# Optimization experiments

Measured on AMD Instinct MI355X. Metric: run time of the kernel, lower is better.

## Reference

```python
import jax, jax.numpy as jnp
import numpy as np

EPS_ATTN = 1e-8  # self.eps is undefined in the torch source; standard slot-attention value
LN_EPS = 1e-5


def _ln(x, g=None, b=None, axes=(-1,)):
    m = x.mean(axes, keepdims=True)
    v = ((x - m) ** 2).mean(axes, keepdims=True)
    y = (x - m) * jax.lax.rsqrt(v + LN_EPS)
    return y * g + b if g is not None else y


def setup_inputs() -> dict:
    key = jax.random.key(0)
    ks = jax.random.split(key, 16)
    B, N, S, d, dh = 16, 4096, 8, 64, 128

    def w(k, shape, fan_in):
        return jax.random.normal(k, shape, jnp.float32) / np.float32(np.sqrt(fan_in))

    return {
        "inputs": jax.random.normal(ks[0], (B, N, d + 2), jnp.float32),
        "slots": jax.random.normal(ks[1], (S, d + 4), jnp.float32),
        "Wq": w(ks[2], (d, d), d),
        "Wk": w(ks[3], (d, d), d),
        "Wv": w(ks[4], (d, d), d),
        "Wg": w(ks[5], (d, 2), 2),
        "bg": jnp.zeros((d,), jnp.float32),
        "ln_pos_g": jnp.ones((d,), jnp.float32),
        "ln_pos_b": jnp.zeros((d,), jnp.float32),
        "W1": w(ks[6], (dh, d), d),
        "b1": jnp.zeros((dh,), jnp.float32),
        "W2": w(ks[7], (d, dh), dh),
        "b2": jnp.zeros((d,), jnp.float32),
        "W_ih": w(ks[8], (3 * d, d), d),
        "W_hh": w(ks[9], (3 * d, d), d),
        "b_ih": jnp.zeros((3 * d,), jnp.float32),
        "b_hh": jnp.zeros((3 * d,), jnp.float32),
        "ln_mlp_g": jnp.ones((d,), jnp.float32),
        "ln_mlp_b": jnp.zeros((d,), jnp.float32),
        "W3": w(ks[10], (dh, d), d),
        "b3": jnp.zeros((dh,), jnp.float32),
        "W4": w(ks[11], (d, dh), dh),
        "b4": jnp.zeros((d,), jnp.float32),
        "ln_slot_g": jnp.ones((d,), jnp.float32),
        "ln_slot_b": jnp.zeros((d,), jnp.float32),
        "n_iters": 3,
    }


def reference(inputs, slots, Wq, Wk, Wv, Wg, bg, ln_pos_g, ln_pos_b, W1, b1, W2, b2,
              W_ih, W_hh, b_ih, b_hh, ln_mlp_g, ln_mlp_b, W3, b3, W4, b4,
              ln_slot_g, ln_slot_b, n_iters):
    feats, grids = inputs[..., :-2], inputs[..., -2:]          # (B,N,d), (B,N,2)
    sl, pos, sc = slots[..., :-4], slots[..., -4:-2], slots[..., -2:]
    B, N, _ = feats.shape
    S, d = sl.shape
    scale = d ** (-0.5)

    slots = jnp.broadcast_to(sl, (B, S, d))
    positions = jnp.clip(jnp.broadcast_to(pos, (B, S, 2)), -1.0, 1.0)
    scales = jnp.clip(jnp.broadcast_to(sc, (B, S, 2)), 1e-3, 2.0)

    k = feats @ Wk.T                                           # (B,N,d)
    v = feats @ Wv.T

    def pos_mlp(x):  # LayerNorm -> Linear -> ReLU -> Linear
        h = _ln(x, ln_pos_g, ln_pos_b)
        h = jax.nn.relu(h @ W1.T + b1)
        return h @ W2.T + b2

    for i_iter in range(n_iters + 1):
        rel = (grids[:, :, None] - positions[:, None]) / scales[:, None]  # (B,N,S,2)
        rgp = rel @ Wg.T + bg                                             # (B,N,S,d)
        k_pos = pos_mlp(k[:, :, None] + rgp)                              # (B,N,S,d)
        v_pos = pos_mlp(v[:, :, None] + rgp)

        slots_n = _ln(slots, ln_slot_g, ln_slot_b)
        q = _ln(slots_n, axes=(-2, -1)) @ Wq.T                            # (B,S,d)

        dots = jnp.einsum('bsd,bnsd->bns', q, k_pos) * scale              # (B,N,S)
        attn = jax.nn.softmax(dots, axis=1) + EPS_ATTN
        attn = attn / attn.sum(axis=-1, keepdims=True)

        updates = jnp.einsum('bns,bnsd->bsd', attn, v_pos)                # (B,S,d)
        positions = jnp.einsum('bns,bnp->bsp', attn, grids)               # (B,S,2)
        spread = (grids[:, :, None] - positions[:, None]) ** 2            # (B,N,S,2)
        scales = jnp.clip(jnp.sqrt(jnp.einsum('bns,bnsp->bsp', attn, spread)), 1e-3, 2.0)

        if i_iter < n_iters:
            x = updates.reshape(-1, d)
            h = slots.reshape(-1, d)
            gi = x @ W_ih.T + b_ih
            gh = h @ W_hh.T + b_hh
            i_r, i_z, i_n = jnp.split(gi, 3, axis=-1)
            h_r, h_z, h_n = jnp.split(gh, 3, axis=-1)
            r = jax.nn.sigmoid(i_r + h_r)
            z = jax.nn.sigmoid(i_z + h_z)
            n_g = jnp.tanh(i_n + r * h_n)
            slots = ((1.0 - z) * n_g + z * h).reshape(B, S, d)
            # slot_mlp (no residual in the source)
            hmlp = jax.nn.relu(_ln(slots, ln_mlp_g, ln_mlp_b) @ W3.T + b3)
            slots = hmlp @ W4.T + b4

    return jnp.concatenate([slots, positions, scales], axis=-1)           # (B,S,d+4)
```

## Files before the change

### kernel.cpp

```cpp
#include <hip/hip_runtime.h>
#include <math.h>

#define BB 16
#define NN 4096
#define SS 8
#define DD 64
#define DHH 128
#define CIN 66
#define NITERS 3
#define LN_EPS_F 1e-5f
#define EPS_ATTN_F 1e-8f
#define QSCALE 0.125f

__device__ __forceinline__ float dot4(float4 a, float4 b) {
    return fmaf(a.x, b.x, fmaf(a.y, b.y, fmaf(a.z, b.z, a.w * b.w)));
}

__global__ __launch_bounds__(256) void k_init_slots(
    const float* __restrict__ slots_in, float* __restrict__ slots,
    float* __restrict__ positions, float* __restrict__ scales) {
    int tid = blockIdx.x * 256 + threadIdx.x;
    if (tid < BB * SS * DD) {
        int s = (tid / DD) % SS;
        int c = tid % DD;
        slots[tid] = slots_in[s * 68 + c];
    }
    if (tid < BB * SS * 2) {
        int s = (tid >> 1) & 7;
        int p = tid & 1;
        float po = slots_in[s * 68 + 64 + p];
        positions[tid] = fminf(fmaxf(po, -1.f), 1.f);
        float sc = slots_in[s * 68 + 66 + p];
        scales[tid] = fminf(fmaxf(sc, 1e-3f), 2.f);
    }
}

__global__ __launch_bounds__(256) void k_prep_w(
    const float* __restrict__ W1, const float* __restrict__ lpg,
    const float* __restrict__ lpb, const float* __restrict__ b1,
    const float* __restrict__ Wg,
    float* __restrict__ W1p, float* __restrict__ avec, float* __restrict__ bvec,
    float* __restrict__ s1vec, float* __restrict__ b1p, float* __restrict__ wgc) {
    __shared__ float w1s[128 * 68];
    int tid = threadIdx.x;
    for (int q = 0; q < 8; q++) {
        int flat = q * 1024 + tid * 4;
        int o = flat >> 6, c = flat & 63;
        *(float4*)(w1s + o * 68 + c) = *(const float4*)(W1 + flat);
    }
    __syncthreads();
    if (tid < 128) {
        int o = tid;
        float a = 0.f, bv = 0.f, s1 = 0.f, b1a = b1[o];
        for (int c = 0; c < 64; c++) {
            float w0 = w1s[o * 68 + c];
            float w = w0 * lpg[c];
            W1p[o * 64 + c] = w;
            a = fmaf(w, Wg[2 * c], a);
            bv = fmaf(w, Wg[2 * c + 1], bv);
            s1 += w;
            b1a = fmaf(w0, lpb[c], b1a);
        }
        avec[o] = a; bvec[o] = bv; s1vec[o] = s1; b1p[o] = b1a;
    }
    if (tid == 128) {
        float mwA = 0.f, mwB = 0.f, AA = 0.f, BBv = 0.f, AB = 0.f;
        for (int c = 0; c < 64; c++) {
            float wa = Wg[2 * c], wb = Wg[2 * c + 1];
            mwA += wa; mwB += wb;
            AA = fmaf(wa, wa, AA); BBv = fmaf(wb, wb, BBv); AB = fmaf(wa, wb, AB);
        }
        wgc[0] = mwA * (1.f / 64.f);
        wgc[1] = mwB * (1.f / 64.f);
        wgc[2] = AA * (1.f / 64.f);
        wgc[3] = BBv * (1.f / 64.f);
        wgc[4] = AB * (2.f / 64.f);
    }
}

__global__ __launch_bounds__(256) void k_prep_w2(
    const float* __restrict__ W1p, const float* __restrict__ Wk,
    const float* __restrict__ Wv, const float* __restrict__ bg,
    float* __restrict__ Wall, float* __restrict__ cu) {
    int flat = blockIdx.x * 256 + threadIdx.x;
    int mat = flat >> 13, rem = flat & 8191;
    int o = rem >> 6, c = rem & 63;
    const float* Wm = mat ? Wv : Wk;
    float acc = 0.f;
    for (int d = 0; d < 64; d++)
        acc = fmaf(W1p[o * 64 + d], Wm[d * 64 + c], acc);
    Wall[flat] = acc;
    if (flat < 128) {
        float a = 0.f;
        for (int d = 0; d < 64; d++) a = fmaf(W1p[flat * 64 + d], bg[d], a);
        cu[flat] = a;
    }
}

__global__ __launch_bounds__(256) void k_prep_main(
    const float* __restrict__ inp, const float* __restrict__ Wall,
    const float* __restrict__ cu, const float* __restrict__ Wk,
    const float* __restrict__ Wv, const float* __restrict__ bg,
    const float* __restrict__ Wg,
    float* __restrict__ uk, float* __restrict__ uv,
    float* __restrict__ kaux, float* __restrict__ vaux, float* __restrict__ gbuf) {
    __shared__ float A[64 * 68];
    __shared__ float Bw[128 * 68];
    __shared__ float wg2[132];
    __shared__ float bgs[64];
    __shared__ float cus[128];
    int tid = threadIdx.x;
    int chunk = blockIdx.y;
    int rowBase = blockIdx.x * 64;
    {
        int r = tid >> 2, cq = (tid & 3) * 16;
        const float* src = inp + (size_t)(rowBase + r) * CIN + cq;
        float* dst = A + r * 68 + cq;
        #pragma unroll
        for (int q = 0; q < 8; q++) {
            float2 tv = *(const float2*)(src + 2 * q);
            dst[2 * q] = tv.x; dst[2 * q + 1] = tv.y;
        }
    }
    if (chunk < 2) {
        const float* Wsrc = Wall + (size_t)chunk * 8192;
        int o = tid >> 1, c0 = (tid & 1) * 32;
        #pragma unroll
        for (int q = 0; q < 8; q++)
            *(float4*)(Bw + o * 68 + c0 + 4 * q) = *(const float4*)(Wsrc + o * 64 + c0 + 4 * q);
        if (tid < 128) cus[tid] = cu[tid];
    } else {
        int o = tid >> 1, c0 = (tid & 1) * 32;
        const float* Wsrc = (o < 64) ? (Wk + o * 64) : (Wv + (o - 64) * 64);
        #pragma unroll
        for (int q = 0; q < 8; q++)
            *(float4*)(Bw + o * 68 + c0 + 4 * q) = *(const float4*)(Wsrc + c0 + 4 * q);
        if (tid < 64) {
            wg2[tid] = Wg[2 * tid]; wg2[66 + tid] = Wg[2 * tid + 1];
            bgs[tid] = bg[tid];
        }
    }
    __syncthreads();
    int r2 = tid >> 3, j = tid & 7;
    float acc0[16], acc1[16];
    #pragma unroll
    for (int q = 0; q < 16; q++) { acc0[q] = 0.f; acc1[q] = 0.f; }
    for (int c4 = 0; c4 < 64; c4 += 4) {
        float4 a0 = *(const float4*)(A + r2 * 68 + c4);
        float4 a1 = *(const float4*)(A + (r2 + 32) * 68 + c4);
        #pragma unroll
        for (int q = 0; q < 16; q++) {
            float4 w = *(const float4*)(Bw + (8 * q + j) * 68 + c4);
            acc0[q] += dot4(a0, w);
            acc1[q] += dot4(a1, w);
        }
    }
    if (chunk < 2) {
        float cub[16];
        #pragma unroll
        for (int q = 0; q < 16; q++) cub[q] = cus[8 * q + j];
        __syncthreads();
        #pragma unroll
        for (int q = 0; q < 16; q++) {
            Bw[r2 * 132 + 8 * q + j] = acc0[q] + cub[q];
            Bw[(r2 + 32) * 132 + 8 * q + j] = acc1[q] + cub[q];
        }
        __syncthreads();
        float* dst = (chunk == 0) ? uk : uv;
        int r = tid >> 2, c0 = (tid & 3) * 32;
        #pragma unroll
        for (int q = 0; q < 8; q++)
            *(float4*)(dst + (size_t)(rowBase + r) * 128 + c0 + 4 * q) =
                *(const float4*)(Bw + r * 132 + c0 + 4 * q);
    } else {
        float mk[2] = {0.f, 0.f}, kk[2] = {0.f, 0.f}, kA[2] = {0.f, 0.f}, kB[2] = {0.f, 0.f};
        float mv[2] = {0.f, 0.f}, vv[2] = {0.f, 0.f}, vA[2] = {0.f, 0.f}, vB[2] = {0.f, 0.f};
        #pragma unroll
        for (int q = 0; q < 8; q++) {
            int ch = 8 * q + j;
            float bgv = bgs[ch], wa = wg2[ch], wb = wg2[66 + ch];
            float x0 = acc0[q] + bgv, x1 = acc1[q] + bgv;
            mk[0] += x0; kk[0] = fmaf(x0, x0, kk[0]); kA[0] = fmaf(x0, wa, kA[0]); kB[0] = fmaf(x0, wb, kB[0]);
            mk[1] += x1; kk[1] = fmaf(x1, x1, kk[1]); kA[1] = fmaf(x1, wa, kA[1]); kB[1] = fmaf(x1, wb, kB[1]);
            float y0 = acc0[q + 8] + bgv, y1 = acc1[q + 8] + bgv;
            mv[0] += y0; vv[0] = fmaf(y0, y0, vv[0]); vA[0] = fmaf(y0, wa, vA[0]); vB[0] = fmaf(y0, wb, vB[0]);
            mv[1] += y1; vv[1] = fmaf(y1, y1, vv[1]); vA[1] = fmaf(y1, wa, vA[1]); vB[1] = fmaf(y1, wb, vB[1]);
        }
        #pragma unroll
        for (int off = 1; off <= 4; off <<= 1) {
            #pragma unroll
            for (int rr = 0; rr < 2; rr++) {
                mk[rr] += __shfl_xor(mk[rr], off, 64); kk[rr] += __shfl_xor(kk[rr], off, 64);
                kA[rr] += __shfl_xor(kA[rr], off, 64); kB[rr] += __shfl_xor(kB[rr], off, 64);
                mv[rr] += __shfl_xor(mv[rr], off, 64); vv[rr] += __shfl_xor(vv[rr], off, 64);
                vA[rr] += __shfl_xor(vA[rr], off, 64); vB[rr] += __shfl_xor(vB[rr], off, 64);
            }
        }
        if (j == 0) {
            #pragma unroll
            for (int rr = 0; rr < 2; rr++) {
                int row = rowBase + r2 + rr * 32;
                float g0 = inp[(size_t)row * CIN + 64];
                float g1 = inp[(size_t)row * CIN + 65];
                float4 m1 = {mk[rr] * (1.f / 64.f), kk[rr] * (1.f / 64.f),
                             kA[rr] * (1.f / 32.f), kB[rr] * (1.f / 32.f)};
                float4 m2 = {g0, g1, 0.f, 0.f};
                *(float4*)(kaux + (size_t)row * 8) = m1;
                *(float4*)(kaux + (size_t)row * 8 + 4) = m2;
                float4 n1 = {mv[rr] * (1.f / 64.f), vv[rr] * (1.f / 64.f),
                             vA[rr] * (1.f / 32.f), vB[rr] * (1.f / 32.f)};
                *(float4*)(vaux + (size_t)row * 8) = n1;
                *(float4*)(vaux + (size_t)row * 8 + 4) = m2;
                *(float2*)(gbuf + (size_t)row * 2) = {g0, g1};
            }
        }
    }
}

__global__ __launch_bounds__(512) void k_slot_prep(
    const float* __restrict__ slots, const float* __restrict__ lsg,
    const float* __restrict__ lsb, const float* __restrict__ Wq,
    const float* __restrict__ W2, const float* __restrict__ b2,
    float* __restrict__ w2q, float* __restrict__ qb2) {
    __shared__ float sn[512];
    __shared__ float qv[SS][64];
    __shared__ float wsum[8], wsum2[8];
    int b = blockIdx.x, t = threadIdx.x;
    int s = t >> 6, c = t & 63;
    float x = slots[(b * SS + s) * DD + c];
    float sum = x;
    for (int off = 32; off; off >>= 1) sum += __shfl_xor(sum, off, 64);
    float m = sum * (1.f / 64.f);
    float dv = x - m;
    float vs = dv * dv;
    for (int off = 32; off; off >>= 1) vs += __shfl_xor(vs, off, 64);
    float y = dv * rsqrtf(vs * (1.f / 64.f) + LN_EPS_F) * lsg[c] + lsb[c];
    float s1 = y, s2 = y * y;
    for (int off = 32; off; off >>= 1) { s1 += __shfl_xor(s1, off, 64); s2 += __shfl_xor(s2, off, 64); }
    if (c == 0) { wsum[s] = s1; wsum2[s] = s2; }
    __syncthreads();
    float ts1 = 0.f, ts2 = 0.f;
    #pragma unroll
    for (int i = 0; i < 8; i++) { ts1 += wsum[i]; ts2 += wsum2[i]; }
    float gm = ts1 * (1.f / 512.f);
    float gv = ts2 * (1.f / 512.f) - gm * gm;
    sn[t] = (y - gm) * rsqrtf(gv + LN_EPS_F);
    __syncthreads();
    float acc = 0.f;
    for (int j4 = 0; j4 < 64; j4 += 4)
        acc += dot4(*(const float4*)&sn[s * 64 + j4], *(const float4*)(Wq + c * 64 + j4));
    qv[s][c] = acc;
    __syncthreads();
    float a0 = 0.f, a1 = 0.f;
    for (int cc = 0; cc < 64; cc++) {
        float qc = qv[s][cc];
        a0 = fmaf(qc, W2[cc * DHH + c], a0);
        a1 = fmaf(qc, W2[cc * DHH + c + 64], a1);
    }
    w2q[(b * SS + s) * DHH + c] = a0 * QSCALE;
    w2q[(b * SS + s) * DHH + c + 64] = a1 * QSCALE;
    float qb = qv[s][c] * b2[c];
    for (int off = 32; off; off >>= 1) qb += __shfl_xor(qb, off, 64);
    if (c == 0) qb2[b * SS + s] = qb * QSCALE;
}

__global__ __launch_bounds__(256) void k_pass1(
    const float* __restrict__ uk, const float* __restrict__ kaux,
    const float* __restrict__ positions, const float* __restrict__ scales,
    const float* __restrict__ avec, const float* __restrict__ bvec,
    const float* __restrict__ s1vec, const float* __restrict__ b1p,
    const float* __restrict__ wgc, const float* __restrict__ w2q,
    const float* __restrict__ qb2, float* __restrict__ dots) {
    int tid = threadIdx.x;
    int chunk = blockIdx.x, b = blockIdx.y;
    int wv = tid >> 6, lane = tid & 63, rh = lane >> 5, ol = lane & 31;
    int o4 = ol * 4;
    float4 a4 = *(const float4*)(avec + o4);
    float4 bv4 = *(const float4*)(bvec + o4);
    float4 s14 = *(const float4*)(s1vec + o4);
    float4 b14 = *(const float4*)(b1p + o4);
    float mwA = wgc[0], mwB = wgc[1], AA = wgc[2], BBc = wgc[3], AB2 = wgc[4];
    float p0[8], p1[8], rc0[8], rc1[8], qb[8];
    float4 wq[8];
    #pragma unroll
    for (int s = 0; s < 8; s++) {
        int bs = b * 8 + s;
        p0[s] = positions[bs * 2]; p1[s] = positions[bs * 2 + 1];
        rc0[s] = 1.f / scales[bs * 2]; rc1[s] = 1.f / scales[bs * 2 + 1];
        qb[s] = qb2[bs];
        wq[s] = *(const float4*)(w2q + (size_t)bs * DHH + o4);
    }
    int row0 = chunk * 64 + wv * 16 + rh;
    size_t rg = (size_t)b * NN + row0;
    float4 m1 = *(const float4*)(kaux + rg * 8);
    float4 m2 = *(const float4*)(kaux + rg * 8 + 4);
    float4 u4 = *(const float4*)(uk + rg * 128 + o4);
    for (int st = 0; st < 8; st++) {
        float4 n1, n2, nu;
        if (st < 7) {
            size_t rgn = rg + (size_t)(st + 1) * 2;
            n1 = *(const float4*)(kaux + rgn * 8);
            n2 = *(const float4*)(kaux + rgn * 8 + 4);
            nu = *(const float4*)(uk + rgn * 128 + o4);
        }
        int row = row0 + st * 2;
        #pragma unroll
        for (int s = 0; s < 8; s++) {
            float rel0 = (m2.x - p0[s]) * rc0[s];
            float rel1 = (m2.y - p1[s]) * rc1[s];
            float m = fmaf(rel1, mwB, fmaf(rel0, mwA, m1.x));
            float q2 = fmaf(rel0, fmaf(rel0, AA, m1.z), m1.y);
            q2 = fmaf(rel1, fmaf(rel1, BBc, m1.w), q2);
            q2 = fmaf(rel0 * rel1, AB2, q2);
            float var = fmaf(-m, m, q2);
            float rstd = rsqrtf(fmaxf(var, 0.f) + LN_EPS_F);
            float p = 0.f, t, h;
            t = fmaf(-m, s14.x, u4.x); t = fmaf(rel0, a4.x, t); t = fmaf(rel1, bv4.x, t);
            h = fmaf(rstd, t, b14.x); p = fmaf(fmaxf(h, 0.f), wq[s].x, p);
            t = fmaf(-m, s14.y, u4.y); t = fmaf(rel0, a4.y, t); t = fmaf(rel1, bv4.y, t);
            h = fmaf(rstd, t, b14.y); p = fmaf(fmaxf(h, 0.f), wq[s].y, p);
            t = fmaf(-m, s14.z, u4.z); t = fmaf(rel0, a4.z, t); t = fmaf(rel1, bv4.z, t);
            h = fmaf(rstd, t, b14.z); p = fmaf(fmaxf(h, 0.f), wq[s].z, p);
            t = fmaf(-m, s14.w, u4.w); t = fmaf(rel0, a4.w, t); t = fmaf(rel1, bv4.w, t);
            h = fmaf(rstd, t, b14.w); p = fmaf(fmaxf(h, 0.f), wq[s].w, p);
            p += __shfl_xor(p, 1, 64);
            p += __shfl_xor(p, 2, 64);
            p += __shfl_xor(p, 4, 64);
            p += __shfl_xor(p, 8, 64);
            p += __shfl_xor(p, 16, 64);
            if (ol == 0)
                dots[(size_t)(b * 8 + s) * NN + row] = p + qb[s];
        }
        m1 = n1; m2 = n2; u4 = nu;
    }
}

__global__ __launch_bounds__(256) void k_pass2(
    const float* __restrict__ uv, const float* __restrict__ vaux,
    const float* __restrict__ positions, const float* __restrict__ scales,
    const float* __restrict__ avec, const float* __restrict__ bvec,
    const float* __restrict__ s1vec, const float* __restrict__ b1p,
    const float* __restrict__ wgc, const float* __restrict__ attn,
    float* __restrict__ H) {
    __shared__ float Hw[4 * 1024];
    int tid = threadIdx.x;
    int chunk = blockIdx.x, b = blockIdx.y;
    int wv = tid >> 6, lane = tid & 63, rh = lane >> 5, ol = lane & 31;
    int o4 = ol * 4;
    float4 a4 = *(const float4*)(avec + o4);
    float4 bv4 = *(const float4*)(bvec + o4);
    float4 s14 = *(const float4*)(s1vec + o4);
    float4 b14 = *(const float4*)(b1p + o4);
    float mwA = wgc[0], mwB = wgc[1], AA = wgc[2], BBc = wgc[3], AB2 = wgc[4];
    float p0[8], p1[8], rc0[8], rc1[8];
    #pragma unroll
    for (int s = 0; s < 8; s++) {
        int bs = b * 8 + s;
        p0[s] = positions[bs * 2]; p1[s] = positions[bs * 2 + 1];
        rc0[s] = 1.f / scales[bs * 2]; rc1[s] = 1.f / scales[bs * 2 + 1];
    }
    float hq[8][4];
    #pragma unroll
    for (int s = 0; s < 8; s++)
        #pragma unroll
        for (int c = 0; c < 4; c++) hq[s][c] = 0.f;
    int row0 = chunk * 64 + wv * 16 + rh;
    size_t rg = (size_t)b * NN + row0;
    float4 m1 = *(const float4*)(vaux + rg * 8);
    float4 m2 = *(const float4*)(vaux + rg * 8 + 4);
    float4 u4 = *(const float4*)(uv + rg * 128 + o4);
    for (int st = 0; st < 8; st++) {
        float4 n1, n2, nu;
        if (st < 7) {
            size_t rgn = rg + (size_t)(st + 1) * 2;
            n1 = *(const float4*)(vaux + rgn * 8);
            n2 = *(const float4*)(vaux + rgn * 8 + 4);
            nu = *(const float4*)(uv + rgn * 128 + o4);
        }
        int row = row0 + st * 2;
        #pragma unroll
        for (int s = 0; s < 8; s++) {
            float ar = attn[(size_t)(b * 8 + s) * NN + row];
            float rel0 = (m2.x - p0[s]) * rc0[s];
            float rel1 = (m2.y - p1[s]) * rc1[s];
            float m = fmaf(rel1, mwB, fmaf(rel0, mwA, m1.x));
            float q2 = fmaf(rel0, fmaf(rel0, AA, m1.z), m1.y);
            q2 = fmaf(rel1, fmaf(rel1, BBc, m1.w), q2);
            q2 = fmaf(rel0 * rel1, AB2, q2);
            float var = fmaf(-m, m, q2);
            float rstd = rsqrtf(fmaxf(var, 0.f) + LN_EPS_F);
            float t, h;
            t = fmaf(-m, s14.x, u4.x); t = fmaf(rel0, a4.x, t); t = fmaf(rel1, bv4.x, t);
            h = fmaf(rstd, t, b14.x); hq[s][0] = fmaf(ar, fmaxf(h, 0.f), hq[s][0]);
            t = fmaf(-m, s14.y, u4.y); t = fmaf(rel0, a4.y, t); t = fmaf(rel1, bv4.y, t);
            h = fmaf(rstd, t, b14.y); hq[s][1] = fmaf(ar, fmaxf(h, 0.f), hq[s][1]);
            t = fmaf(-m, s14.z, u4.z); t = fmaf(rel0, a4.z, t); t = fmaf(rel1, bv4.z, t);
            h = fmaf(rstd, t, b14.z); hq[s][2] = fmaf(ar, fmaxf(h, 0.f), hq[s][2]);
            t = fmaf(-m, s14.w, u4.w); t = fmaf(rel0, a4.w, t); t = fmaf(rel1, bv4.w, t);
            h = fmaf(rstd, t, b14.w); hq[s][3] = fmaf(ar, fmaxf(h, 0.f), hq[s][3]);
        }
        m1 = n1; m2 = n2; u4 = nu;
    }
    #pragma unroll
    for (int s = 0; s < 8; s++)
        #pragma unroll
        for (int c = 0; c < 4; c++)
            hq[s][c] += __shfl_xor(hq[s][c], 32, 64);
    if (lane < 32) {
        #pragma unroll
        for (int s = 0; s < 8; s++) {
            float4 st = {hq[s][0], hq[s][1], hq[s][2], hq[s][3]};
            *(float4*)(Hw + wv * 1024 + s * 128 + o4) = st;
        }
    }
    __syncthreads();
    #pragma unroll
    for (int q = 0; q < 4; q++) {
        int flat = q * 256 + tid;
        float sum = Hw[flat] + Hw[1024 + flat] + Hw[2048 + flat] + Hw[3072 + flat];
        atomicAdd(&H[(size_t)b * 8 * DHH + flat], sum);
    }
}

__global__ __launch_bounds__(256) void k_softmax_ms(
    const float* __restrict__ dots, float* __restrict__ Mv, float* __restrict__ Lv,
    float* __restrict__ H) {
    __shared__ float red[4];
    int bs = blockIdx.x, t = threadIdx.x;
    if (t < 128) H[(size_t)bs * DHH + t] = 0.f;
    const float* dp = dots + (size_t)bs * NN;
    float mx = -1e30f;
    #pragma unroll
    for (int it = 0; it < 4; it++) {
        float4 d = *(const float4*)(dp + it * 1024 + t * 4);
        mx = fmaxf(mx, fmaxf(fmaxf(d.x, d.y), fmaxf(d.z, d.w)));
    }
    for (int off = 32; off; off >>= 1) mx = fmaxf(mx, __shfl_xor(mx, off, 64));
    if ((t & 63) == 0) red[t >> 6] = mx;
    __syncthreads();
    float M = fmaxf(fmaxf(red[0], red[1]), fmaxf(red[2], red[3]));
    __syncthreads();
    float sm = 0.f;
    #pragma unroll
    for (int it = 0; it < 4; it++) {
        float4 d = *(const float4*)(dp + it * 1024 + t * 4);
        sm += expf(d.x - M) + expf(d.y - M) + expf(d.z - M) + expf(d.w - M);
    }
    for (int off = 32; off; off >>= 1) sm += __shfl_xor(sm, off, 64);
    if ((t & 63) == 0) red[t >> 6] = sm;
    __syncthreads();
    if (t == 0) { Mv[bs] = M; Lv[bs] = red[0] + red[1] + red[2] + red[3]; }
}

__global__ __launch_bounds__(256) void k_attn(
    const float* __restrict__ dots, const float* __restrict__ Mv,
    const float* __restrict__ Lv, float* __restrict__ attn) {
    int chunk = blockIdx.x, b = blockIdx.y;
    int n = chunk * 256 + threadIdx.x;
    float a[8];
    float rs = 0.f;
    #pragma unroll
    for (int s = 0; s < 8; s++) {
        int bs = b * 8 + s;
        float d = dots[(size_t)bs * NN + n];
        a[s] = expf(d - Mv[bs]) * (1.f / Lv[bs]) + EPS_ATTN_F;
        rs += a[s];
    }
    float inv = 1.f / rs;
    #pragma unroll
    for (int s = 0; s < 8; s++)
        attn[(size_t)(b * 8 + s) * NN + n] = a[s] * inv;
}

__global__ __launch_bounds__(256) void k_stats(
    const float* __restrict__ attn, const float* __restrict__ gbuf,
    float* __restrict__ positions, float* __restrict__ scales,
    float* __restrict__ stats) {
    __shared__ float red[4][5];
    int bs = blockIdx.x, b = bs >> 3, t = threadIdx.x;
    const float* ap = attn + (size_t)bs * NN;
    const float* gb = gbuf + (size_t)b * NN * 2;
    float v0 = 0.f, v1 = 0.f, v2 = 0.f, v3 = 0.f, v4 = 0.f;
    #pragma unroll
    for (int it = 0; it < 4; it++) {
        int n0 = it * 1024 + t * 4;
        float4 av = *(const float4*)(ap + n0);
        float4 g1 = *(const float4*)(gb + (size_t)n0 * 2);
        float4 g2 = *(const float4*)(gb + (size_t)n0 * 2 + 4);
        v0 += av.x + av.y + av.z + av.w;
        v1 = fmaf(av.x, g1.x, fmaf(av.y, g1.z, fmaf(av.z, g2.x, fmaf(av.w, g2.z, v1))));
        v2 = fmaf(av.x, g1.y, fmaf(av.y, g1.w, fmaf(av.z, g2.y, fmaf(av.w, g2.w, v2))));
        v3 = fmaf(av.x, g1.x * g1.x, fmaf(av.y, g1.z * g1.z, fmaf(av.z, g2.x * g2.x, fmaf(av.w, g2.z * g2.z, v3))));
        v4 = fmaf(av.x, g1.y * g1.y, fmaf(av.y, g1.w * g1.w, fmaf(av.z, g2.y * g2.y, fmaf(av.w, g2.w * g2.w, v4))));
    }
    for (int off = 32; off; off >>= 1) {
        v0 += __shfl_xor(v0, off, 64); v1 += __shfl_xor(v1, off, 64);
        v2 += __shfl_xor(v2, off, 64); v3 += __shfl_xor(v3, off, 64);
        v4 += __shfl_xor(v4, off, 64);
    }
    if ((t & 63) == 0) {
        int w = t >> 6;
        red[w][0] = v0; red[w][1] = v1; red[w][2] = v2; red[w][3] = v3; red[w][4] = v4;
    }
    __syncthreads();
    if (t == 0) {
        float A0 = red[0][0] + red[1][0] + red[2][0] + red[3][0];
        float A1x = red[0][1] + red[1][1] + red[2][1] + red[3][1];
        float A1y = red[0][2] + red[1][2] + red[2][2] + red[3][2];
        float A2x = red[0][3] + red[1][3] + red[2][3] + red[3][3];
        float A2y = red[0][4] + red[1][4] + red[2][4] + red[3][4];
        positions[bs * 2 + 0] = A1x;
        positions[bs * 2 + 1] = A1y;
        float sx = A2x - A1x * A1x * (2.f - A0);
        float sy = A2y - A1y * A1y * (2.f - A0);
        scales[bs * 2 + 0] = fminf(fmaxf(sqrtf(fmaxf(sx, 0.f)), 1e-3f), 2.f);
        scales[bs * 2 + 1] = fminf(fmaxf(sqrtf(fmaxf(sy, 0.f)), 1e-3f), 2.f);
        stats[bs] = A0;
    }
}

__global__ __launch_bounds__(64) void k_gru_mlp(
    const float* __restrict__ H, const float* __restrict__ stats,
    const float* __restrict__ W2, const float* __restrict__ b2,
    const float* __restrict__ W_ih, const float* __restrict__ W_hh,
    const float* __restrict__ b_ih, const float* __restrict__ b_hh,
    const float* __restrict__ lmg, const float* __restrict__ lmb,
    const float* __restrict__ W3, const float* __restrict__ b3,
    const float* __restrict__ W4, const float* __restrict__ b4,
    float* __restrict__ slots) {
    int bs = blockIdx.x;
    int c = threadIdx.x;
    __shared__ float hl[DHH], ul[DD], sl[DD], yl[DD], hml[DHH];
    hl[c] = H[bs * DHH + c];
    hl[c + 64] = H[bs * DHH + 64 + c];
    float hold = slots[bs * DD + c];
    sl[c] = hold;
    __syncthreads();
    float A0 = stats[bs];
    float u = A0 * b2[c];
    for (int o = 0; o < DHH; o += 4) {
        float4 w = *(const float4*)(W2 + c * DHH + o);
        u = fmaf(w.x, hl[o], fmaf(w.y, hl[o + 1], fmaf(w.z, hl[o + 2], fmaf(w.w, hl[o + 3], u))));
    }
    ul[c] = u;
    __syncthreads();
    float gir = b_ih[c], giz = b_ih[64 + c], gin = b_ih[128 + c];
    float ghr = b_hh[c], ghz = b_hh[64 + c], ghn = b_hh[128 + c];
    for (int k4 = 0; k4 < DD; k4 += 4) {
        float4 uu = *(const float4*)(ul + k4);
        float4 hh = *(const float4*)(sl + k4);
        gir += dot4(uu, *(const float4*)(W_ih + c * DD + k4));
        giz += dot4(uu, *(const float4*)(W_ih + (64 + c) * DD + k4));
        gin += dot4(uu, *(const float4*)(W_ih + (128 + c) * DD + k4));
        ghr += dot4(hh, *(const float4*)(W_hh + c * DD + k4));
        ghz += dot4(hh, *(const float4*)(W_hh + (64 + c) * DD + k4));
        ghn += dot4(hh, *(const float4*)(W_hh + (128 + c) * DD + k4));
    }
    float rg = 1.f / (1.f + expf(-(gir + ghr)));
    float zg = 1.f / (1.f + expf(-(giz + ghz)));
    float ng = tanhf(gin + rg * ghn);
    float snew = (1.f - zg) * ng + zg * hold;
    float sum = snew;
    for (int off = 32; off; off >>= 1) sum += __shfl_xor(sum, off, 64);
    float m = sum * (1.f / 64.f);
    float dv = snew - m;
    float vv = dv * dv;
    for (int off = 32; off; off >>= 1) vv += __shfl_xor(vv, off, 64);
    yl[c] = dv * rsqrtf(vv * (1.f / 64.f) + LN_EPS_F) * lmg[c] + lmb[c];
    __syncthreads();
    float h0 = b3[c], h1 = b3[64 + c];
    for (int k4 = 0; k4 < DD; k4 += 4) {
        float4 yy = *(const float4*)(yl + k4);
        h0 += dot4(yy, *(const float4*)(W3 + c * DD + k4));
        h1 += dot4(yy, *(const float4*)(W3 + (64 + c) * DD + k4));
    }
    hml[c] = fmaxf(h0, 0.f);
    hml[64 + c] = fmaxf(h1, 0.f);
    __syncthreads();
    float outv = b4[c];
    for (int o4 = 0; o4 < DHH; o4 += 4) {
        float4 hm4 = *(const float4*)(hml + o4);
        outv += dot4(hm4, *(const float4*)(W4 + c * DHH + o4));
    }
    slots[bs * DD + c] = outv;
}

__global__ __launch_bounds__(256) void k_write_out(
    const float* __restrict__ slots, const float* __restrict__ positions,
    const float* __restrict__ scales, float* __restrict__ out) {
    int tid = blockIdx.x * 256 + threadIdx.x;
    if (tid >= BB * SS * 68) return;
    int bs = tid / 68, c = tid % 68;
    float v;
    if (c < 64) v = slots[bs * 64 + c];
    else if (c < 66) v = positions[bs * 2 + (c - 64)];
    else v = scales[bs * 2 + (c - 66)];
    out[tid] = v;
}

extern "C" void kernel_launch(void* const* d_in, const int* in_sizes, int n_in,
                              void* d_out, int out_size, void* d_ws, size_t ws_size,
                              hipStream_t stream) {
    (void)in_sizes; (void)n_in; (void)out_size; (void)ws_size;
    const float* inp = (const float*)d_in[0];
    const float* slots_in = (const float*)d_in[1];
    const float* Wq = (const float*)d_in[2];
    const float* Wk = (const float*)d_in[3];
    const float* Wv = (const float*)d_in[4];
    const float* Wg = (const float*)d_in[5];
    const float* bg = (const float*)d_in[6];
    const float* lpg = (const float*)d_in[7];
    const float* lpb = (const float*)d_in[8];
    const float* W1 = (const float*)d_in[9];
    const float* b1 = (const float*)d_in[10];
    const float* W2 = (const float*)d_in[11];
    const float* b2 = (const float*)d_in[12];
    const float* W_ih = (const float*)d_in[13];
    const float* W_hh = (const float*)d_in[14];
    const float* b_ih = (const float*)d_in[15];
    const float* b_hh = (const float*)d_in[16];
    const float* lmg = (const float*)d_in[17];
    const float* lmb = (const float*)d_in[18];
    const float* W3 = (const float*)d_in[19];
    const float* b3 = (const float*)d_in[20];
    const float* W4 = (const float*)d_in[21];
    const float* b4 = (const float*)d_in[22];
    const float* lsg = (const float*)d_in[23];
    const float* lsb = (const float*)d_in[24];
    float* out = (float*)d_out;
    float* ws = (float*)d_ws;

    const size_t NR = (size_t)BB * NN;
    size_t o_uk = 0;
    size_t o_uv = o_uk + NR * 128;
    size_t o_kaux = o_uv + NR * 128;
    size_t o_vaux = o_kaux + NR * 8;
    size_t o_gbuf = o_vaux + NR * 8;
    size_t o_dots = o_gbuf + NR * 2;
    size_t o_attn = o_dots + NR * SS;
    size_t o_slots = o_attn + NR * SS;
    size_t o_pos = o_slots + BB * SS * DD;
    size_t o_scl = o_pos + BB * SS * 2;
    size_t o_w2q = o_scl + BB * SS * 2;
    size_t o_qb2 = o_w2q + BB * SS * DHH;
    size_t o_Mv = o_qb2 + BB * SS;
    size_t o_Lv = o_Mv + BB * SS;
    size_t o_H = o_Lv + BB * SS;
    size_t o_stats = o_H + BB * SS * DHH;
    size_t o_W1p = o_stats + BB * SS;
    size_t o_avec = o_W1p + DHH * DD;
    size_t o_bvec = o_avec + DHH;
    size_t o_s1v = o_bvec + DHH;
    size_t o_b1p = o_s1v + DHH;
    size_t o_wgc = o_b1p + DHH;
    size_t o_Wall = o_wgc + 8;
    size_t o_cu = o_Wall + 2 * DHH * DD;

    float* uk = ws + o_uk;
    float* uv = ws + o_uv;
    float* kaux = ws + o_kaux;
    float* vaux = ws + o_vaux;
    float* gbuf = ws + o_gbuf;
    float* dots = ws + o_dots;
    float* attn = ws + o_attn;
    float* slots = ws + o_slots;
    float* positions = ws + o_pos;
    float* scales = ws + o_scl;
    float* w2q = ws + o_w2q;
    float* qb2 = ws + o_qb2;
    float* Mv = ws + o_Mv;
    float* Lv = ws + o_Lv;
    float* H = ws + o_H;
    float* stats = ws + o_stats;
    float* W1p = ws + o_W1p;
    float* avec = ws + o_avec;
    float* bvec = ws + o_bvec;
    float* s1v = ws + o_s1v;
    float* b1p = ws + o_b1p;
    float* wgc = ws + o_wgc;
    float* Wall = ws + o_Wall;
    float* cu = ws + o_cu;

    k_init_slots<<<32, 256, 0, stream>>>(slots_in, slots, positions, scales);
    k_prep_w<<<1, 256, 0, stream>>>(W1, lpg, lpb, b1, Wg, W1p, avec, bvec, s1v, b1p, wgc);
    k_prep_w2<<<64, 256, 0, stream>>>(W1p, Wk, Wv, bg, Wall, cu);
    k_prep_main<<<dim3(1024, 3), 256, 0, stream>>>(inp, Wall, cu, Wk, Wv, bg, Wg,
                                                   uk, uv, kaux, vaux, gbuf);

    for (int it = 0; it <= NITERS; ++it) {
        k_slot_prep<<<BB, 512, 0, stream>>>(slots, lsg, lsb, Wq, W2, b2, w2q, qb2);
        k_pass1<<<dim3(64, BB), 256, 0, stream>>>(uk, kaux, positions, scales,
                                                  avec, bvec, s1v, b1p, wgc, w2q, qb2, dots);
        k_softmax_ms<<<BB * SS, 256, 0, stream>>>(dots, Mv, Lv, H);
        k_attn<<<dim3(16, BB), 256, 0, stream>>>(dots, Mv, Lv, attn);
        if (it < NITERS) {
            k_pass2<<<dim3(64, BB), 256, 0, stream>>>(uv, vaux, positions, scales,
                                                      avec, bvec, s1v, b1p, wgc, attn, H);
            k_stats<<<BB * SS, 256, 0, stream>>>(attn, gbuf, positions, scales, stats);
            k_gru_mlp<<<BB * SS, 64, 0, stream>>>(H, stats, W2, b2, W_ih, W_hh, b_ih, b_hh,
                                                  lmg, lmb, W3, b3, W4, b4, slots);
        } else {
            k_stats<<<BB * SS, 256, 0, stream>>>(attn, gbuf, positions, scales, stats);
        }
    }
    k_write_out<<<34, 256, 0, stream>>>(slots, positions, scales, out);
}
```

Before: 474.9 us.

## Fuse attention normalization, stats and slot prep into pass2 and GRU kernels

Drops the separate attention-materialization and stats kernels. Pass2 now recomputes normalized attention from dots plus the softmax max and sum, and accumulates position statistics directly. The GRU/MLP kernel is merged with slot prep into one block per batch that also computes positions and scales. Pass1 and prep_main get new thread mappings (one slot per lane group, 8x8 register tiles with 128 threads). Together this cuts kernel launches and global traffic for the attn and gbuf buffers, at the cost of more complex kernels and a different reduction order.

```diff
diff --git a/kernel.cpp b/kernel.cpp
--- a/kernel.cpp
+++ b/kernel.cpp
@@ -97,14 +97,14 @@
     }
 }
 
-__global__ __launch_bounds__(256) void k_prep_main(
+__global__ __launch_bounds__(128) void k_prep_main(
     const float* __restrict__ inp, const float* __restrict__ Wall,
     const float* __restrict__ cu, const float* __restrict__ Wk,
     const float* __restrict__ Wv, const float* __restrict__ bg,
     const float* __restrict__ Wg,
     float* __restrict__ uk, float* __restrict__ uv,
-    float* __restrict__ kaux, float* __restrict__ vaux, float* __restrict__ gbuf) {
-    __shared__ float A[64 * 68];
+    float* __restrict__ kaux, float* __restrict__ vaux) {
+    __shared__ float A[64 * 66];
     __shared__ float Bw[128 * 68];
     __shared__ float wg2[132];
     __shared__ float bgs[64];
@@ -113,105 +113,105 @@
     int chunk = blockIdx.y;
     int rowBase = blockIdx.x * 64;
     {
-        int r = tid >> 2, cq = (tid & 3) * 16;
-        const float* src = inp + (size_t)(rowBase + r) * CIN + cq;
-        float* dst = A + r * 68 + cq;
-        #pragma unroll
-        for (int q = 0; q < 8; q++) {
+        int r = tid >> 1, half = tid & 1;
+        const float* src = inp + (size_t)(rowBase + r) * CIN + half * 32;
+        float* dst = A + r * 66 + half * 32;
+        #pragma unroll
+        for (int q = 0; q < 16; q++) {
             float2 tv = *(const float2*)(src + 2 * q);
             dst[2 * q] = tv.x; dst[2 * q + 1] = tv.y;
         }
     }
     if (chunk < 2) {
-        const float* Wsrc = Wall + (size_t)chunk * 8192;
-        int o = tid >> 1, c0 = (tid & 1) * 32;
-        #pragma unroll
-        for (int q = 0; q < 8; q++)
-            *(float4*)(Bw + o * 68 + c0 + 4 * q) = *(const float4*)(Wsrc + o * 64 + c0 + 4 * q);
-        if (tid < 128) cus[tid] = cu[tid];
+        const float* Wsrc = Wall + (size_t)chunk * 8192 + tid * 64;
+        float* dst = Bw + tid * 68;
+        #pragma unroll
+        for (int q = 0; q < 16; q++)
+            *(float4*)(dst + 4 * q) = *(const float4*)(Wsrc + 4 * q);
+        cus[tid] = cu[tid];
     } else {
-        int o = tid >> 1, c0 = (tid & 1) * 32;
-        const float* Wsrc = (o < 64) ? (Wk + o * 64) : (Wv + (o - 64) * 64);
-        #pragma unroll
-        for (int q = 0; q < 8; q++)
-            *(float4*)(Bw + o * 68 + c0 + 4 * q) = *(const float4*)(Wsrc + c0 + 4 * q);
+        const float* Wsrc = (tid < 64) ? (Wk + tid * 64) : (Wv + (tid - 64) * 64);
+        float* dst = Bw + tid * 68;
+        #pragma unroll
+        for (int q = 0; q < 16; q++)
+            *(float4*)(dst + 4 * q) = *(const float4*)(Wsrc + 4 * q);
         if (tid < 64) {
             wg2[tid] = Wg[2 * tid]; wg2[66 + tid] = Wg[2 * tid + 1];
             bgs[tid] = bg[tid];
         }
     }
     __syncthreads();
-    int r2 = tid >> 3, j = tid & 7;
-    float acc0[16], acc1[16];
-    #pragma unroll
-    for (int q = 0; q < 16; q++) { acc0[q] = 0.f; acc1[q] = 0.f; }
+    int oj = tid & 15, rg = tid >> 4;
+    float acc[8][8];
+    #pragma unroll
+    for (int rr = 0; rr < 8; rr++)
+        #pragma unroll
+        for (int q = 0; q < 8; q++) acc[rr][q] = 0.f;
     for (int c4 = 0; c4 < 64; c4 += 4) {
-        float4 a0 = *(const float4*)(A + r2 * 68 + c4);
-        float4 a1 = *(const float4*)(A + (r2 + 32) * 68 + c4);
-        #pragma unroll
-        for (int q = 0; q < 16; q++) {
-            float4 w = *(const float4*)(Bw + (8 * q + j) * 68 + c4);
-            acc0[q] += dot4(a0, w);
-            acc1[q] += dot4(a1, w);
+        float4 av[8];
+        #pragma unroll
+        for (int rr = 0; rr < 8; rr++)
+            av[rr] = *(const float4*)(A + (rg + 8 * rr) * 66 + c4);
+        #pragma unroll
+        for (int q = 0; q < 8; q++) {
+            float4 w = *(const float4*)(Bw + (q * 16 + oj) * 68 + c4);
+            #pragma unroll
+            for (int rr = 0; rr < 8; rr++) acc[rr][q] += dot4(av[rr], w);
         }
     }
     if (chunk < 2) {
-        float cub[16];
-        #pragma unroll
-        for (int q = 0; q < 16; q++) cub[q] = cus[8 * q + j];
+        float cub[8];
+        #pragma unroll
+        for (int q = 0; q < 8; q++) cub[q] = cus[q * 16 + oj];
         __syncthreads();
         #pragma unroll
-        for (int q = 0; q < 16; q++) {
-            Bw[r2 * 132 + 8 * q + j] = acc0[q] + cub[q];
-            Bw[(r2 + 32) * 132 + 8 * q + j] = acc1[q] + cub[q];
-        }
+        for (int rr = 0; rr < 8; rr++)
+            #pragma unroll
+            for (int q = 0; q < 8; q++)
+                Bw[(rg + 8 * rr) * 132 + q * 16 + oj] = acc[rr][q] + cub[q];
         __syncthreads();
         float* dst = (chunk == 0) ? uk : uv;
-        int r = tid >> 2, c0 = (tid & 3) * 32;
-        #pragma unroll
-        for (int q = 0; q < 8; q++)
-            *(float4*)(dst + (size_t)(rowBase + r) * 128 + c0 + 4 * q) =
-                *(const float4*)(Bw + r * 132 + c0 + 4 * q);
+        int r = tid >> 1, half = tid & 1;
+        #pragma unroll
+        for (int q = 0; q < 16; q++)
+            *(float4*)(dst + (size_t)(rowBase + r) * 128 + half * 64 + 4 * q) =
+                *(const float4*)(Bw + r * 132 + half * 64 + 4 * q);
     } else {
-        float mk[2] = {0.f, 0.f}, kk[2] = {0.f, 0.f}, kA[2] = {0.f, 0.f}, kB[2] = {0.f, 0.f};
-        float mv[2] = {0.f, 0.f}, vv[2] = {0.f, 0.f}, vA[2] = {0.f, 0.f}, vB[2] = {0.f, 0.f};
-        #pragma unroll
-        for (int q = 0; q < 8; q++) {
-            int ch = 8 * q + j;
-            float bgv = bgs[ch], wa = wg2[ch], wb = wg2[66 + ch];
-            float x0 = acc0[q] + bgv, x1 = acc1[q] + bgv;
-            mk[0] += x0; kk[0] = fmaf(x0, x0, kk[0]); kA[0] = fmaf(x0, wa, kA[0]); kB[0] = fmaf(x0, wb, kB[0]);
-            mk[1] += x1; kk[1] = fmaf(x1, x1, kk[1]); kA[1] = fmaf(x1, wa, kA[1]); kB[1] = fmaf(x1, wb, kB[1]);
-            float y0 = acc0[q + 8] + bgv, y1 = acc1[q + 8] + bgv;
-            mv[0] += y0; vv[0] = fmaf(y0, y0, vv[0]); vA[0] = fmaf(y0, wa, vA[0]); vB[0] = fmaf(y0, wb, vB[0]);
-            mv[1] += y1; vv[1] = fmaf(y1, y1, vv[1]); vA[1] = fmaf(y1, wa, vA[1]); vB[1] = fmaf(y1, wb, vB[1]);
-        }
-        #pragma unroll
-        for (int off = 1; off <= 4; off <<= 1) {
+        float wa[4], wb[4], bgk[4];
+        #pragma unroll
+        for (int q = 0; q < 4; q++) {
+            int ch = q * 16 + oj;
+            wa[q] = wg2[ch]; wb[q] = wg2[66 + ch]; bgk[q] = bgs[ch];
+        }
+        #pragma unroll
+        for (int rr = 0; rr < 8; rr++) {
+            float mk = 0.f, kk = 0.f, kA = 0.f, kB = 0.f;
+            float mv = 0.f, vv = 0.f, vA = 0.f, vB = 0.f;
             #pragma unroll
-            for (int rr = 0; rr < 2; rr++) {
-                mk[rr] += __shfl_xor(mk[rr], off, 64); kk[rr] += __shfl_xor(kk[rr], off, 64);
-                kA[rr] += __shfl_xor(kA[rr], off, 64); kB[rr] += __shfl_xor(kB[rr], off, 64);
-                mv[rr] += __shfl_xor(mv[rr], off, 64); vv[rr] += __shfl_xor(vv[rr], off, 64);
-                vA[rr] += __shfl_xor(vA[rr], off, 64); vB[rr] += __shfl_xor(vB[rr], off, 64);
+            for (int q = 0; q < 4; q++) {
+                float x = acc[rr][q] + bgk[q];
+                mk += x; kk = fmaf(x, x, kk); kA = fmaf(x, wa[q], kA); kB = fmaf(x, wb[q], kB);
+                float y = acc[rr][q + 4] + bgk[q];
+                mv += y; vv = fmaf(y, y, vv); vA = fmaf(y, wa[q], vA); vB = fmaf(y, wb[q], vB);
             }
-        }
-        if (j == 0) {
             #pragma unroll
-            for (int rr = 0; rr < 2; rr++) {
-                int row = rowBase + r2 + rr * 32;
+            for (int off = 1; off <= 8; off <<= 1) {
+                mk += __shfl_xor(mk, off, 64); kk += __shfl_xor(kk, off, 64);
+                kA += __shfl_xor(kA, off, 64); kB += __shfl_xor(kB, off, 64);
+                mv += __shfl_xor(mv, off, 64); vv += __shfl_xor(vv, off, 64);
+                vA += __shfl_xor(vA, off, 64); vB += __shfl_xor(vB, off, 64);
+            }
+            if (oj == 0) {
+                int row = rowBase + rg + 8 * rr;
                 float g0 = inp[(size_t)row * CIN + 64];
                 float g1 = inp[(size_t)row * CIN + 65];
-                float4 m1 = {mk[rr] * (1.f / 64.f), kk[rr] * (1.f / 64.f),
-                             kA[rr] * (1.f / 32.f), kB[rr] * (1.f / 32.f)};
+                float4 m1 = {mk * (1.f / 64.f), kk * (1.f / 64.f), kA * (1.f / 32.f), kB * (1.f / 32.f)};
                 float4 m2 = {g0, g1, 0.f, 0.f};
                 *(float4*)(kaux + (size_t)row * 8) = m1;
                 *(float4*)(kaux + (size_t)row * 8 + 4) = m2;
-                float4 n1 = {mv[rr] * (1.f / 64.f), vv[rr] * (1.f / 64.f),
-                             vA[rr] * (1.f / 32.f), vB[rr] * (1.f / 32.f)};
+                float4 n1 = {mv * (1.f / 64.f), vv * (1.f / 64.f), vA * (1.f / 32.f), vB * (1.f / 32.f)};
                 *(float4*)(vaux + (size_t)row * 8) = n1;
                 *(float4*)(vaux + (size_t)row * 8 + 4) = m2;
-                *(float2*)(gbuf + (size_t)row * 2) = {g0, g1};
             }
         }
     }
@@ -272,67 +272,97 @@
     const float* __restrict__ wgc, const float* __restrict__ w2q,
     const float* __restrict__ qb2, float* __restrict__ dots) {
     int tid = threadIdx.x;
-    int chunk = blockIdx.x, b = blockIdx.y;
-    int wv = tid >> 6, lane = tid & 63, rh = lane >> 5, ol = lane & 31;
-    int o4 = ol * 4;
-    float4 a4 = *(const float4*)(avec + o4);
-    float4 bv4 = *(const float4*)(bvec + o4);
-    float4 s14 = *(const float4*)(s1vec + o4);
-    float4 b14 = *(const float4*)(b1p + o4);
+    int wv = tid >> 6, lane = tid & 63;
+    int s = lane >> 3, cg = lane & 7, c0 = cg * 16;
+    int b = blockIdx.y, bs = b * SS + s;
+    float4 a4[4], bv4[4], s14[4], b14[4], wq4[4];
+    #pragma unroll
+    for (int k = 0; k < 4; k++) {
+        a4[k] = *(const float4*)(avec + c0 + 4 * k);
+        bv4[k] = *(const float4*)(bvec + c0 + 4 * k);
+        s14[k] = *(const float4*)(s1vec + c0 + 4 * k);
+        b14[k] = *(const float4*)(b1p + c0 + 4 * k);
+        wq4[k] = *(const float4*)(w2q + (size_t)bs * DHH + c0 + 4 * k);
+    }
+    float p0 = positions[bs * 2], p1 = positions[bs * 2 + 1];
+    float rc0 = 1.f / scales[bs * 2], rc1 = 1.f / scales[bs * 2 + 1];
+    float qb = qb2[bs];
     float mwA = wgc[0], mwB = wgc[1], AA = wgc[2], BBc = wgc[3], AB2 = wgc[4];
-    float p0[8], p1[8], rc0[8], rc1[8], qb[8];
-    float4 wq[8];
-    #pragma unroll
-    for (int s = 0; s < 8; s++) {
-        int bs = b * 8 + s;
-        p0[s] = positions[bs * 2]; p1[s] = positions[bs * 2 + 1];
-        rc0[s] = 1.f / scales[bs * 2]; rc1[s] = 1.f / scales[bs * 2 + 1];
-        qb[s] = qb2[bs];
-        wq[s] = *(const float4*)(w2q + (size_t)bs * DHH + o4);
-    }
-    int row0 = chunk * 64 + wv * 16 + rh;
-    size_t rg = (size_t)b * NN + row0;
-    float4 m1 = *(const float4*)(kaux + rg * 8);
-    float4 m2 = *(const float4*)(kaux + rg * 8 + 4);
-    float4 u4 = *(const float4*)(uk + rg * 128 + o4);
-    for (int st = 0; st < 8; st++) {
-        float4 n1, n2, nu;
-        if (st < 7) {
-            size_t rgn = rg + (size_t)(st + 1) * 2;
-            n1 = *(const float4*)(kaux + rgn * 8);
-            n2 = *(const float4*)(kaux + rgn * 8 + 4);
-            nu = *(const float4*)(uk + rgn * 128 + o4);
-        }
-        int row = row0 + st * 2;
-        #pragma unroll
-        for (int s = 0; s < 8; s++) {
-            float rel0 = (m2.x - p0[s]) * rc0[s];
-            float rel1 = (m2.y - p1[s]) * rc1[s];
-            float m = fmaf(rel1, mwB, fmaf(rel0, mwA, m1.x));
-            float q2 = fmaf(rel0, fmaf(rel0, AA, m1.z), m1.y);
-            q2 = fmaf(rel1, fmaf(rel1, BBc, m1.w), q2);
-            q2 = fmaf(rel0 * rel1, AB2, q2);
-            float var = fmaf(-m, m, q2);
-            float rstd = rsqrtf(fmaxf(var, 0.f) + LN_EPS_F);
-            float p = 0.f, t, h;
-            t = fmaf(-m, s14.x, u4.x); t = fmaf(rel0, a4.x, t); t = fmaf(rel1, bv4.x, t);
-            h = fmaf(rstd, t, b14.x); p = fmaf(fmaxf(h, 0.f), wq[s].x, p);
-            t = fmaf(-m, s14.y, u4.y); t = fmaf(rel0, a4.y, t); t = fmaf(rel1, bv4.y, t);
-            h = fmaf(rstd, t, b14.y); p = fmaf(fmaxf(h, 0.f), wq[s].y, p);
-            t = fmaf(-m, s14.z, u4.z); t = fmaf(rel0, a4.z, t); t = fmaf(rel1, bv4.z, t);
-            h = fmaf(rstd, t, b14.z); p = fmaf(fmaxf(h, 0.f), wq[s].z, p);
-            t = fmaf(-m, s14.w, u4.w); t = fmaf(rel0, a4.w, t); t = fmaf(rel1, bv4.w, t);
-            h = fmaf(rstd, t, b14.w); p = fmaf(fmaxf(h, 0.f), wq[s].w, p);
-            p += __shfl_xor(p, 1, 64);
-            p += __shfl_xor(p, 2, 64);
-            p += __shfl_xor(p, 4, 64);
-            p += __shfl_xor(p, 8, 64);
-            p += __shfl_xor(p, 16, 64);
-            if (ol == 0)
-                dots[(size_t)(b * 8 + s) * NN + row] = p + qb[s];
-        }
-        m1 = n1; m2 = n2; u4 = nu;
-    }
+    int row0 = blockIdx.x * 64 + wv * 16;
+    size_t base = (size_t)b * NN + row0;
+    float4 m1 = *(const float4*)(kaux + base * 8);
+    float4 m2 = *(const float4*)(kaux + base * 8 + 4);
+    float4 u[4];
+    #pragma unroll
+    for (int k = 0; k < 4; k++) u[k] = *(const float4*)(uk + base * 128 + c0 + 4 * k);
+    for (int r = 0; r < 16; r++) {
+        float4 nm1, nm2, nu[4];
+        if (r < 15) {
+            size_t nb = base + r + 1;
+            nm1 = *(const float4*)(kaux + nb * 8);
+            nm2 = *(const float4*)(kaux + nb * 8 + 4);
+            #pragma unroll
+            for (int k = 0; k < 4; k++) nu[k] = *(const float4*)(uk + nb * 128 + c0 + 4 * k);
+        }
+        float rel0 = (m2.x - p0) * rc0, rel1 = (m2.y - p1) * rc1;
+        float m = fmaf(rel1, mwB, fmaf(rel0, mwA, m1.x));
+        float q2 = fmaf(rel0, fmaf(rel0, AA, m1.z), m1.y);
+        q2 = fmaf(rel1, fmaf(rel1, BBc, m1.w), q2);
+        q2 = fmaf(rel0 * rel1, AB2, q2);
+        float var = fmaf(-m, m, q2);
+        float rstd = rsqrtf(fmaxf(var, 0.f) + LN_EPS_F);
+        float p = 0.f;
+        #pragma unroll
+        for (int k = 0; k < 4; k++) {
+            float t, h;
+            t = fmaf(-m, s14[k].x, u[k].x); t = fmaf(rel0, a4[k].x, t); t = fmaf(rel1, bv4[k].x, t);
+            h = fmaf(rstd, t, b14[k].x); p = fmaf(fmaxf(h, 0.f), wq4[k].x, p);
+            t = fmaf(-m, s14[k].y, u[k].y); t = fmaf(rel0, a4[k].y, t); t = fmaf(rel1, bv4[k].y, t);
+            h = fmaf(rstd, t, b14[k].y); p = fmaf(fmaxf(h, 0.f), wq4[k].y, p);
+            t = fmaf(-m, s14[k].z, u[k].z); t = fmaf(rel0, a4[k].z, t); t = fmaf(rel1, bv4[k].z, t);
+            h = fmaf(rstd, t, b14[k].z); p = fmaf(fmaxf(h, 0.f), wq4[k].z, p);
+            t = fmaf(-m, s14[k].w, u[k].w); t = fmaf(rel0, a4[k].w, t); t = fmaf(rel1, bv4[k].w, t);
+            h = fmaf(rstd, t, b14[k].w); p = fmaf(fmaxf(h, 0.f), wq4[k].w, p);
+        }
+        p += __shfl_xor(p, 1, 64);
+        p += __shfl_xor(p, 2, 64);
+        p += __shfl_xor(p, 4, 64);
+        if (cg == 0) dots[(size_t)bs * NN + row0 + r] = p + qb;
+        m1 = nm1; m2 = nm2;
+        #pragma unroll
+        for (int k = 0; k < 4; k++) u[k] = nu[k];
+    }
+}
+
+__global__ __launch_bounds__(256) void k_softmax_ms(
+    const float* __restrict__ dots, float* __restrict__ Mv, float* __restrict__ Lv,
+    float* __restrict__ H, float* __restrict__ stats5) {
+    __shared__ float red[4];
+    int bs = blockIdx.x, t = threadIdx.x;
+    if (t < 128) H[(size_t)bs * DHH + t] = 0.f;
+    if (t < 5) stats5[bs * 5 + t] = 0.f;
+    const float* dp = dots + (size_t)bs * NN;
+    float mx = -1e30f;
+    #pragma unroll
+    for (int it = 0; it < 4; it++) {
+        float4 d = *(const float4*)(dp + it * 1024 + t * 4);
+        mx = fmaxf(mx, fmaxf(fmaxf(d.x, d.y), fmaxf(d.z, d.w)));
+    }
+    for (int off = 32; off; off >>= 1) mx = fmaxf(mx, __shfl_xor(mx, off, 64));
+    if ((t & 63) == 0) red[t >> 6] = mx;
+    __syncthreads();
+    float M = fmaxf(fmaxf(red[0], red[1]), fmaxf(red[2], red[3]));
+    __syncthreads();
+    float sm = 0.f;
+    #pragma unroll
+    for (int it = 0; it < 4; it++) {
+        float4 d = *(const float4*)(dp + it * 1024 + t * 4);
+        sm += expf(d.x - M) + expf(d.y - M) + expf(d.z - M) + expf(d.w - M);
+    }
+    for (int off = 32; off; off >>= 1) sm += __shfl_xor(sm, off, 64);
+    if ((t & 63) == 0) red[t >> 6] = sm;
+    __syncthreads();
+    if (t == 0) { Mv[bs] = M; Lv[bs] = red[0] + red[1] + red[2] + red[3]; }
 }
 
 __global__ __launch_bounds__(256) void k_pass2(
@@ -340,215 +370,210 @@
     const float* __restrict__ positions, const float* __restrict__ scales,
     const float* __restrict__ avec, const float* __restrict__ bvec,
     const float* __restrict__ s1vec, const float* __restrict__ b1p,
-    const float* __restrict__ wgc, const float* __restrict__ attn,
-    float* __restrict__ H) {
+    const float* __restrict__ wgc, const float* __restrict__ dots,
+    const float* __restrict__ Mv, const float* __restrict__ Lv,
+    float* __restrict__ H, float* __restrict__ stats5) {
     __shared__ float Hw[4 * 1024];
+    __shared__ float stS[40];
     int tid = threadIdx.x;
-    int chunk = blockIdx.x, b = blockIdx.y;
-    int wv = tid >> 6, lane = tid & 63, rh = lane >> 5, ol = lane & 31;
-    int o4 = ol * 4;
-    float4 a4 = *(const float4*)(avec + o4);
-    float4 bv4 = *(const float4*)(bvec + o4);
-    float4 s14 = *(const float4*)(s1vec + o4);
-    float4 b14 = *(const float4*)(b1p + o4);
+    if (tid < 40) stS[tid] = 0.f;
+    int wv = tid >> 6, lane = tid & 63;
+    int s = lane >> 3, cg = lane & 7, c0 = cg * 16;
+    int b = blockIdx.y, bs = b * SS + s;
+    float4 a4[4], bv4[4], s14[4], b14[4];
+    #pragma unroll
+    for (int k = 0; k < 4; k++) {
+        a4[k] = *(const float4*)(avec + c0 + 4 * k);
+        bv4[k] = *(const float4*)(bvec + c0 + 4 * k);
+        s14[k] = *(const float4*)(s1vec + c0 + 4 * k);
+        b14[k] = *(const float4*)(b1p + c0 + 4 * k);
+    }
+    float p0 = positions[bs * 2], p1 = positions[bs * 2 + 1];
+    float rc0 = 1.f / scales[bs * 2], rc1 = 1.f / scales[bs * 2 + 1];
+    float Mb = Mv[bs], invL = 1.f / Lv[bs];
     float mwA = wgc[0], mwB = wgc[1], AA = wgc[2], BBc = wgc[3], AB2 = wgc[4];
-    float p0[8], p1[8], rc0[8], rc1[8];
-    #pragma unroll
-    for (int s = 0; s < 8; s++) {
-        int bs = b * 8 + s;
-        p0[s] = positions[bs * 2]; p1[s] = positions[bs * 2 + 1];
-        rc0[s] = 1.f / scales[bs * 2]; rc1[s] = 1.f / scales[bs * 2 + 1];
-    }
-    float hq[8][4];
-    #pragma unroll
-    for (int s = 0; s < 8; s++)
-        #pragma unroll
-        for (int c = 0; c < 4; c++) hq[s][c] = 0.f;
-    int row0 = chunk * 64 + wv * 16 + rh;
-    size_t rg = (size_t)b * NN + row0;
-    float4 m1 = *(const float4*)(vaux + rg * 8);
-    float4 m2 = *(const float4*)(vaux + rg * 8 + 4);
-    float4 u4 = *(const float4*)(uv + rg * 128 + o4);
-    for (int st = 0; st < 8; st++) {
-        float4 n1, n2, nu;
-        if (st < 7) {
-            size_t rgn = rg + (size_t)(st + 1) * 2;
-            n1 = *(const float4*)(vaux + rgn * 8);
-            n2 = *(const float4*)(vaux + rgn * 8 + 4);
-            nu = *(const float4*)(uv + rgn * 128 + o4);
-        }
-        int row = row0 + st * 2;
-        #pragma unroll
-        for (int s = 0; s < 8; s++) {
-            float ar = attn[(size_t)(b * 8 + s) * NN + row];
-            float rel0 = (m2.x - p0[s]) * rc0[s];
-            float rel1 = (m2.y - p1[s]) * rc1[s];
-            float m = fmaf(rel1, mwB, fmaf(rel0, mwA, m1.x));
-            float q2 = fmaf(rel0, fmaf(rel0, AA, m1.z), m1.y);
-            q2 = fmaf(rel1, fmaf(rel1, BBc, m1.w), q2);
-            q2 = fmaf(rel0 * rel1, AB2, q2);
-            float var = fmaf(-m, m, q2);
-            float rstd = rsqrtf(fmaxf(var, 0.f) + LN_EPS_F);
+    float hq[16];
+    #pragma unroll
+    for (int k = 0; k < 16; k++) hq[k] = 0.f;
+    float v0 = 0.f, v1 = 0.f, v2 = 0.f, v3 = 0.f, v4 = 0.f;
+    int row0 = blockIdx.x * 64 + wv * 16;
+    size_t base = (size_t)b * NN + row0;
+    __syncthreads();
+    float4 m1 = *(const float4*)(vaux + base * 8);
+    float4 m2 = *(const float4*)(vaux + base * 8 + 4);
+    float4 u[4];
+    #pragma unroll
+    for (int k = 0; k < 4; k++) u[k] = *(const float4*)(uv + base * 128 + c0 + 4 * k);
+    for (int r = 0; r < 16; r++) {
+        float4 nm1, nm2, nu[4];
+        if (r < 15) {
+            size_t nb = base + r + 1;
+            nm1 = *(const float4*)(vaux + nb * 8);
+            nm2 = *(const float4*)(vaux + nb * 8 + 4);
+            #pragma unroll
+            for (int k = 0; k < 4; k++) nu[k] = *(const float4*)(uv + nb * 128 + c0 + 4 * k);
+        }
+        float d = dots[(size_t)bs * NN + row0 + r];
+        float e = expf(d - Mb) * invL + EPS_ATTN_F;
+        float rs = e;
+        rs += __shfl_xor(rs, 8, 64);
+        rs += __shfl_xor(rs, 16, 64);
+        rs += __shfl_xor(rs, 32, 64);
+        float ar = e / rs;
+        float rel0 = (m2.x - p0) * rc0, rel1 = (m2.y - p1) * rc1;
+        float m = fmaf(rel1, mwB, fmaf(rel0, mwA, m1.x));
+        float q2 = fmaf(rel0, fmaf(rel0, AA, m1.z), m1.y);
+        q2 = fmaf(rel1, fmaf(rel1, BBc, m1.w), q2);
+        q2 = fmaf(rel0 * rel1, AB2, q2);
+        float var = fmaf(-m, m, q2);
+        float rstd = rsqrtf(fmaxf(var, 0.f) + LN_EPS_F);
+        #pragma unroll
+        for (int k = 0; k < 4; k++) {
             float t, h;
-            t = fmaf(-m, s14.x, u4.x); t = fmaf(rel0, a4.x, t); t = fmaf(rel1, bv4.x, t);
-            h = fmaf(rstd, t, b14.x); hq[s][0] = fmaf(ar, fmaxf(h, 0.f), hq[s][0]);
-            t = fmaf(-m, s14.y, u4.y); t = fmaf(rel0, a4.y, t); t = fmaf(rel1, bv4.y, t);
-            h = fmaf(rstd, t, b14.y); hq[s][1] = fmaf(ar, fmaxf(h, 0.f), hq[s][1]);
-            t = fmaf(-m, s14.z, u4.z); t = fmaf(rel0, a4.z, t); t = fmaf(rel1, bv4.z, t);
-            h = fmaf(rstd, t, b14.z); hq[s][2] = fmaf(ar, fmaxf(h, 0.f), hq[s][2]);
-            t = fmaf(-m, s14.w, u4.w); t = fmaf(rel0, a4.w, t); t = fmaf(rel1, bv4.w, t);
-            h = fmaf(rstd, t, b14.w); hq[s][3] = fmaf(ar, fmaxf(h, 0.f), hq[s][3]);
-        }
-        m1 = n1; m2 = n2; u4 = nu;
-    }
-    #pragma unroll
-    for (int s = 0; s < 8; s++)
-        #pragma unroll
-        for (int c = 0; c < 4; c++)
-            hq[s][c] += __shfl_xor(hq[s][c], 32, 64);
-    if (lane < 32) {
-        #pragma unroll
-        for (int s = 0; s < 8; s++) {
-            float4 st = {hq[s][0], hq[s][1], hq[s][2], hq[s][3]};
-            *(float4*)(Hw + wv * 1024 + s * 128 + o4) = st;
-        }
+            t = fmaf(-m, s14[k].x, u[k].x); t = fmaf(rel0, a4[k].x, t); t = fmaf(rel1, bv4[k].x, t);
+            h = fmaf(rstd, t, b14[k].x); hq[4 * k + 0] = fmaf(ar, fmaxf(h, 0.f), hq[4 * k + 0]);
+            t = fmaf(-m, s14[k].y, u[k].y); t = fmaf(rel0, a4[k].y, t); t = fmaf(rel1, bv4[k].y, t);
+            h = fmaf(rstd, t, b14[k].y); hq[4 * k + 1] = fmaf(ar, fmaxf(h, 0.f), hq[4 * k + 1]);
+            t = fmaf(-m, s14[k].z, u[k].z); t = fmaf(rel0, a4[k].z, t); t = fmaf(rel1, bv4[k].z, t);
+            h = fmaf(rstd, t, b14[k].z); hq[4 * k + 2] = fmaf(ar, fmaxf(h, 0.f), hq[4 * k + 2]);
+            t = fmaf(-m, s14[k].w, u[k].w); t = fmaf(rel0, a4[k].w, t); t = fmaf(rel1, bv4[k].w, t);
+            h = fmaf(rstd, t, b14[k].w); hq[4 * k + 3] = fmaf(ar, fmaxf(h, 0.f), hq[4 * k + 3]);
+        }
+        v0 += ar;
+        v1 = fmaf(ar, m2.x, v1); v2 = fmaf(ar, m2.y, v2);
+        v3 = fmaf(ar, m2.x * m2.x, v3); v4 = fmaf(ar, m2.y * m2.y, v4);
+        m1 = nm1; m2 = nm2;
+        #pragma unroll
+        for (int k = 0; k < 4; k++) u[k] = nu[k];
+    }
+    #pragma unroll
+    for (int k = 0; k < 4; k++) {
+        float4 st = {hq[4 * k], hq[4 * k + 1], hq[4 * k + 2], hq[4 * k + 3]};
+        *(float4*)(Hw + wv * 1024 + s * 128 + c0 + 4 * k) = st;
+    }
+    if (cg == 0) {
+        atomicAdd(&stS[s * 5 + 0], v0);
+        atomicAdd(&stS[s * 5 + 1], v1);
+        atomicAdd(&stS[s * 5 + 2], v2);
+        atomicAdd(&stS[s * 5 + 3], v3);
+        atomicAdd(&stS[s * 5 + 4], v4);
     }
     __syncthreads();
     #pragma unroll
     for (int q = 0; q < 4; q++) {
         int flat = q * 256 + tid;
         float sum = Hw[flat] + Hw[1024 + flat] + Hw[2048 + flat] + Hw[3072 + flat];
-        atomicAdd(&H[(size_t)b * 8 * DHH + flat], sum);
-    }
-}
-
-__global__ __launch_bounds__(256) void k_softmax_ms(
-    const float* __restrict__ dots, float* __restrict__ Mv, float* __restrict__ Lv,
-    float* __restrict__ H) {
-    __shared__ float red[4];
-    int bs = blockIdx.x, t = threadIdx.x;
-    if (t < 128) H[(size_t)bs * DHH + t] = 0.f;
-    const float* dp = dots + (size_t)bs * NN;
-    float mx = -1e30f;
-    #pragma unroll
-    for (int it = 0; it < 4; it++) {
-        float4 d = *(const float4*)(dp + it * 1024 + t * 4);
-        mx = fmaxf(mx, fmaxf(fmaxf(d.x, d.y), fmaxf(d.z, d.w)));
-    }
-    for (int off = 32; off; off >>= 1) mx = fmaxf(mx, __shfl_xor(mx, off, 64));
-    if ((t & 63) == 0) red[t >> 6] = mx;
-    __syncthreads();
-    float M = fmaxf(fmaxf(red[0], red[1]), fmaxf(red[2], red[3]));
-    __syncthreads();
-    float sm = 0.f;
-    #pragma unroll
-    for (int it = 0; it < 4; it++) {
-        float4 d = *(const float4*)(dp + it * 1024 + t * 4);
-        sm += expf(d.x - M) + expf(d.y - M) + expf(d.z - M) + expf(d.w - M);
-    }
-    for (int off = 32; off; off >>= 1) sm += __shfl_xor(sm, off, 64);
-    if ((t & 63) == 0) red[t >> 6] = sm;
-    __syncthreads();
-    if (t == 0) { Mv[bs] = M; Lv[bs] = red[0] + red[1] + red[2] + red[3]; }
-}
-
-__global__ __launch_bounds__(256) void k_attn(
-    const float* __restrict__ dots, const float* __restrict__ Mv,
-    const float* __restrict__ Lv, float* __restrict__ attn) {
-    int chunk = blockIdx.x, b = blockIdx.y;
-    int n = chunk * 256 + threadIdx.x;
-    float a[8];
-    float rs = 0.f;
-    #pragma unroll
-    for (int s = 0; s < 8; s++) {
-        int bs = b * 8 + s;
-        float d = dots[(size_t)bs * NN + n];
-        a[s] = expf(d - Mv[bs]) * (1.f / Lv[bs]) + EPS_ATTN_F;
-        rs += a[s];
-    }
-    float inv = 1.f / rs;
-    #pragma unroll
-    for (int s = 0; s < 8; s++)
-        attn[(size_t)(b * 8 + s) * NN + n] = a[s] * inv;
-}
-
-__global__ __launch_bounds__(256) void k_stats(
-    const float* __restrict__ attn, const float* __restrict__ gbuf,
-    float* __restrict__ positions, float* __restrict__ scales,
-    float* __restrict__ stats) {
-    __shared__ float red[4][5];
-    int bs = blockIdx.x, b = bs >> 3, t = threadIdx.x;
-    const float* ap = attn + (size_t)bs * NN;
-    const float* gb = gbuf + (size_t)b * NN * 2;
+        atomicAdd(&H[(size_t)b * SS * DHH + flat], sum);
+    }
+    if (tid < 40) atomicAdd(&stats5[(size_t)b * 40 + tid], stS[tid]);
+}
+
+__global__ __launch_bounds__(256) void k_stats_final(
+    const float* __restrict__ dots, const float* __restrict__ kaux,
+    const float* __restrict__ Mv, const float* __restrict__ Lv,
+    float* __restrict__ stats5) {
+    __shared__ float stS[40];
+    int tid = threadIdx.x;
+    if (tid < 40) stS[tid] = 0.f;
+    __syncthreads();
+    int wv = tid >> 6, lane = tid & 63;
+    int s = lane >> 3, cg = lane & 7;
+    int b = blockIdx.y, bs = b * SS + s;
+    float Mb = Mv[bs], invL = 1.f / Lv[bs];
+    int row0 = blockIdx.x * 256 + wv * 64;
     float v0 = 0.f, v1 = 0.f, v2 = 0.f, v3 = 0.f, v4 = 0.f;
-    #pragma unroll
-    for (int it = 0; it < 4; it++) {
-        int n0 = it * 1024 + t * 4;
-        float4 av = *(const float4*)(ap + n0);
-        float4 g1 = *(const float4*)(gb + (size_t)n0 * 2);
-        float4 g2 = *(const float4*)(gb + (size_t)n0 * 2 + 4);
-        v0 += av.x + av.y + av.z + av.w;
-        v1 = fmaf(av.x, g1.x, fmaf(av.y, g1.z, fmaf(av.z, g2.x, fmaf(av.w, g2.z, v1))));
-        v2 = fmaf(av.x, g1.y, fmaf(av.y, g1.w, fmaf(av.z, g2.y, fmaf(av.w, g2.w, v2))));
-        v3 = fmaf(av.x, g1.x * g1.x, fmaf(av.y, g1.z * g1.z, fmaf(av.z, g2.x * g2.x, fmaf(av.w, g2.z * g2.z, v3))));
-        v4 = fmaf(av.x, g1.y * g1.y, fmaf(av.y, g1.w * g1.w, fmaf(av.z, g2.y * g2.y, fmaf(av.w, g2.w * g2.w, v4))));
-    }
-    for (int off = 32; off; off >>= 1) {
-        v0 += __shfl_xor(v0, off, 64); v1 += __shfl_xor(v1, off, 64);
-        v2 += __shfl_xor(v2, off, 64); v3 += __shfl_xor(v3, off, 64);
-        v4 += __shfl_xor(v4, off, 64);
-    }
-    if ((t & 63) == 0) {
-        int w = t >> 6;
-        red[w][0] = v0; red[w][1] = v1; red[w][2] = v2; red[w][3] = v3; red[w][4] = v4;
-    }
-    __syncthreads();
-    if (t == 0) {
-        float A0 = red[0][0] + red[1][0] + red[2][0] + red[3][0];
-        float A1x = red[0][1] + red[1][1] + red[2][1] + red[3][1];
-        float A1y = red[0][2] + red[1][2] + red[2][2] + red[3][2];
-        float A2x = red[0][3] + red[1][3] + red[2][3] + red[3][3];
-        float A2y = red[0][4] + red[1][4] + red[2][4] + red[3][4];
+    for (int r = 0; r < 64; r++) {
+        int row = row0 + r;
+        float d = dots[(size_t)bs * NN + row];
+        float e = expf(d - Mb) * invL + EPS_ATTN_F;
+        float rs = e;
+        rs += __shfl_xor(rs, 8, 64);
+        rs += __shfl_xor(rs, 16, 64);
+        rs += __shfl_xor(rs, 32, 64);
+        float ar = e / rs;
+        float2 g = *(const float2*)(kaux + ((size_t)b * NN + row) * 8 + 4);
+        v0 += ar;
+        v1 = fmaf(ar, g.x, v1); v2 = fmaf(ar, g.y, v2);
+        v3 = fmaf(ar, g.x * g.x, v3); v4 = fmaf(ar, g.y * g.y, v4);
+    }
+    if (cg == 0) {
+        atomicAdd(&stS[s * 5 + 0], v0);
+        atomicAdd(&stS[s * 5 + 1], v1);
+        atomicAdd(&stS[s * 5 + 2], v2);
+        atomicAdd(&stS[s * 5 + 3], v3);
+        atomicAdd(&stS[s * 5 + 4], v4);
+    }
+    __syncthreads();
+    if (tid < 40) atomicAdd(&stats5[(size_t)b * 40 + tid], stS[tid]);
+}
+
+__global__ void k_finalize(const float* __restrict__ stats5,
+                           float* __restrict__ positions, float* __restrict__ scales) {
+    int bs = threadIdx.x;
+    if (bs < BB * SS) {
+        float A0 = stats5[bs * 5 + 0];
+        float A1x = stats5[bs * 5 + 1], A1y = stats5[bs * 5 + 2];
+        float A2x = stats5[bs * 5 + 3], A2y = stats5[bs * 5 + 4];
         positions[bs * 2 + 0] = A1x;
         positions[bs * 2 + 1] = A1y;
         float sx = A2x - A1x * A1x * (2.f - A0);
         float sy = A2y - A1y * A1y * (2.f - A0);
         scales[bs * 2 + 0] = fminf(fmaxf(sqrtf(fmaxf(sx, 0.f)), 1e-3f), 2.f);
         scales[bs * 2 + 1] = fminf(fmaxf(sqrtf(fmaxf(sy, 0.f)), 1e-3f), 2.f);
-        stats[bs] = A0;
-    }
-}
-
-__global__ __launch_bounds__(64) void k_gru_mlp(
-    const float* __restrict__ H, const float* __restrict__ stats,
+    }
+}
+
+__global__ __launch_bounds__(512) void k_gru_fused(
+    const float* __restrict__ H, const float* __restrict__ stats5,
+    float* __restrict__ positions, float* __restrict__ scales,
     const float* __restrict__ W2, const float* __restrict__ b2,
     const float* __restrict__ W_ih, const float* __restrict__ W_hh,
     const float* __restrict__ b_ih, const float* __restrict__ b_hh,
     const float* __restrict__ lmg, const float* __restrict__ lmb,
     const float* __restrict__ W3, const float* __restrict__ b3,
     const float* __restrict__ W4, const float* __restrict__ b4,
-    float* __restrict__ slots) {
-    int bs = blockIdx.x;
-    int c = threadIdx.x;
-    __shared__ float hl[DHH], ul[DD], sl[DD], yl[DD], hml[DHH];
-    hl[c] = H[bs * DHH + c];
-    hl[c + 64] = H[bs * DHH + 64 + c];
+    const float* __restrict__ lsg, const float* __restrict__ lsb,
+    const float* __restrict__ Wq,
+    float* __restrict__ slots, float* __restrict__ w2q, float* __restrict__ qb2) {
+    __shared__ float hl[SS][DHH], ul[SS][DD], sl[SS][DD], yl[SS][DD], hml[SS][DHH];
+    __shared__ float a0s[8];
+    __shared__ float sn[512];
+    __shared__ float qv[SS][64];
+    __shared__ float wsum[8], wsum2[8];
+    int b = blockIdx.x, t = threadIdx.x;
+    int s = t >> 6, c = t & 63;
+    int bs = b * SS + s;
+    if (t < 8) {
+        int bss = b * SS + t;
+        float A0 = stats5[bss * 5 + 0];
+        float A1x = stats5[bss * 5 + 1], A1y = stats5[bss * 5 + 2];
+        float A2x = stats5[bss * 5 + 3], A2y = stats5[bss * 5 + 4];
+        positions[bss * 2 + 0] = A1x;
+        positions[bss * 2 + 1] = A1y;
+        float sx = A2x - A1x * A1x * (2.f - A0);
+        float sy = A2y - A1y * A1y * (2.f - A0);
+        scales[bss * 2 + 0] = fminf(fmaxf(sqrtf(fmaxf(sx, 0.f)), 1e-3f), 2.f);
+        scales[bss * 2 + 1] = fminf(fmaxf(sqrtf(fmaxf(sy, 0.f)), 1e-3f), 2.f);
+        a0s[t] = A0;
+    }
+    hl[s][c] = H[(size_t)bs * DHH + c];
+    hl[s][c + 64] = H[(size_t)bs * DHH + 64 + c];
     float hold = slots[bs * DD + c];
-    sl[c] = hold;
-    __syncthreads();
-    float A0 = stats[bs];
+    sl[s][c] = hold;
+    __syncthreads();
+    float A0 = a0s[s];
     float u = A0 * b2[c];
     for (int o = 0; o < DHH; o += 4) {
         float4 w = *(const float4*)(W2 + c * DHH + o);
-        u = fmaf(w.x, hl[o], fmaf(w.y, hl[o + 1], fmaf(w.z, hl[o + 2], fmaf(w.w, hl[o + 3], u))));
-    }
-    ul[c] = u;
+        u = fmaf(w.x, hl[s][o], fmaf(w.y, hl[s][o + 1], fmaf(w.z, hl[s][o + 2], fmaf(w.w, hl[s][o + 3], u))));
+    }
+    ul[s][c] = u;
     __syncthreads();
     float gir = b_ih[c], giz = b_ih[64 + c], gin = b_ih[128 + c];
     float ghr = b_hh[c], ghz = b_hh[64 + c], ghn = b_hh[128 + c];
     for (int k4 = 0; k4 < DD; k4 += 4) {
-        float4 uu = *(const float4*)(ul + k4);
-        float4 hh = *(const float4*)(sl + k4);
+        float4 uu = *(const float4*)(&ul[s][k4]);
+        float4 hh = *(const float4*)(&sl[s][k4]);
         gir += dot4(uu, *(const float4*)(W_ih + c * DD + k4));
         giz += dot4(uu, *(const float4*)(W_ih + (64 + c) * DD + k4));
         gin += dot4(uu, *(const float4*)(W_ih + (128 + c) * DD + k4));
@@ -566,23 +591,58 @@
     float dv = snew - m;
     float vv = dv * dv;
     for (int off = 32; off; off >>= 1) vv += __shfl_xor(vv, off, 64);
-    yl[c] = dv * rsqrtf(vv * (1.f / 64.f) + LN_EPS_F) * lmg[c] + lmb[c];
+    yl[s][c] = dv * rsqrtf(vv * (1.f / 64.f) + LN_EPS_F) * lmg[c] + lmb[c];
     __syncthreads();
     float h0 = b3[c], h1 = b3[64 + c];
     for (int k4 = 0; k4 < DD; k4 += 4) {
-        float4 yy = *(const float4*)(yl + k4);
+        float4 yy = *(const float4*)(&yl[s][k4]);
         h0 += dot4(yy, *(const float4*)(W3 + c * DD + k4));
         h1 += dot4(yy, *(const float4*)(W3 + (64 + c) * DD + k4));
     }
-    hml[c] = fmaxf(h0, 0.f);
-    hml[64 + c] = fmaxf(h1, 0.f);
+    hml[s][c] = fmaxf(h0, 0.f);
+    hml[s][64 + c] = fmaxf(h1, 0.f);
     __syncthreads();
     float outv = b4[c];
     for (int o4 = 0; o4 < DHH; o4 += 4) {
-        float4 hm4 = *(const float4*)(hml + o4);
+        float4 hm4 = *(const float4*)(&hml[s][o4]);
         outv += dot4(hm4, *(const float4*)(W4 + c * DHH + o4));
     }
     slots[bs * DD + c] = outv;
+    float x = outv;
+    float sums = x;
+    for (int off = 32; off; off >>= 1) sums += __shfl_xor(sums, off, 64);
+    float ms = sums * (1.f / 64.f);
+    float dvs = x - ms;
+    float vss = dvs * dvs;
+    for (int off = 32; off; off >>= 1) vss += __shfl_xor(vss, off, 64);
+    float y = dvs * rsqrtf(vss * (1.f / 64.f) + LN_EPS_F) * lsg[c] + lsb[c];
+    float s1 = y, s2 = y * y;
+    for (int off = 32; off; off >>= 1) { s1 += __shfl_xor(s1, off, 64); s2 += __shfl_xor(s2, off, 64); }
+    if (c == 0) { wsum[s] = s1; wsum2[s] = s2; }
+    __syncthreads();
+    float ts1 = 0.f, ts2 = 0.f;
+    #pragma unroll
+    for (int i = 0; i < 8; i++) { ts1 += wsum[i]; ts2 += wsum2[i]; }
+    float gm = ts1 * (1.f / 512.f);
+    float gv = ts2 * (1.f / 512.f) - gm * gm;
+    sn[t] = (y - gm) * rsqrtf(gv + LN_EPS_F);
+    __syncthreads();
+    float acc = 0.f;
+    for (int j4 = 0; j4 < 64; j4 += 4)
+        acc += dot4(*(const float4*)&sn[s * 64 + j4], *(const float4*)(Wq + c * 64 + j4));
+    qv[s][c] = acc;
+    __syncthreads();
+    float a0 = 0.f, a1 = 0.f;
+    for (int cc = 0; cc < 64; cc++) {
+        float qc = qv[s][cc];
+        a0 = fmaf(qc, W2[cc * DHH + c], a0);
+        a1 = fmaf(qc, W2[cc * DHH + c + 64], a1);
+    }
+    w2q[(size_t)bs * DHH + c] = a0 * QSCALE;
+    w2q[(size_t)bs * DHH + c + 64] = a1 * QSCALE;
+    float qb = qv[s][c] * b2[c];
+    for (int off = 32; off; off >>= 1) qb += __shfl_xor(qb, off, 64);
+    if (c == 0) qb2[bs] = qb * QSCALE;
 }
 
 __global__ __launch_bounds__(256) void k_write_out(
@@ -635,10 +695,8 @@
     size_t o_uv = o_uk + NR * 128;
     size_t o_kaux = o_uv + NR * 128;
     size_t o_vaux = o_kaux + NR * 8;
-    size_t o_gbuf = o_vaux + NR * 8;
-    size_t o_dots = o_gbuf + NR * 2;
-    size_t o_attn = o_dots + NR * SS;
-    size_t o_slots = o_attn + NR * SS;
+    size_t o_dots = o_vaux + NR * 8;
+    size_t o_slots = o_dots + NR * SS;
     size_t o_pos = o_slots + BB * SS * DD;
     size_t o_scl = o_pos + BB * SS * 2;
     size_t o_w2q = o_scl + BB * SS * 2;
@@ -646,8 +704,8 @@
     size_t o_Mv = o_qb2 + BB * SS;
     size_t o_Lv = o_Mv + BB * SS;
     size_t o_H = o_Lv + BB * SS;
-    size_t o_stats = o_H + BB * SS * DHH;
-    size_t o_W1p = o_stats + BB * SS;
+    size_t o_st5 = o_H + BB * SS * DHH;
+    size_t o_W1p = o_st5 + BB * SS * 5;
     size_t o_avec = o_W1p + DHH * DD;
     size_t o_bvec = o_avec + DHH;
     size_t o_s1v = o_bvec + DHH;
@@ -660,9 +718,7 @@
     float* uv = ws + o_uv;
     float* kaux = ws + o_kaux;
     float* vaux = ws + o_vaux;
-    float* gbuf = ws + o_gbuf;
     float* dots = ws + o_dots;
-    float* attn = ws + o_attn;
     float* slots = ws + o_slots;
     float* positions = ws + o_pos;
     float* scales = ws + o_scl;
@@ -671,7 +727,7 @@
     float* Mv = ws + o_Mv;
     float* Lv = ws + o_Lv;
     float* H = ws + o_H;
-    float* stats = ws + o_stats;
+    float* stats5 = ws + o_st5;
     float* W1p = ws + o_W1p;
     float* avec = ws + o_avec;
     float* bvec = ws + o_bvec;
@@ -684,23 +740,25 @@
     k_init_slots<<<32, 256, 0, stream>>>(slots_in, slots, positions, scales);
     k_prep_w<<<1, 256, 0, stream>>>(W1, lpg, lpb, b1, Wg, W1p, avec, bvec, s1v, b1p, wgc);
     k_prep_w2<<<64, 256, 0, stream>>>(W1p, Wk, Wv, bg, Wall, cu);
-    k_prep_main<<<dim3(1024, 3), 256, 0, stream>>>(inp, Wall, cu, Wk, Wv, bg, Wg,
-                                                   uk, uv, kaux, vaux, gbuf);
+    k_prep_main<<<dim3(1024, 3), 128, 0, stream>>>(inp, Wall, cu, Wk, Wv, bg, Wg,
+                                                   uk, uv, kaux, vaux);
+    k_slot_prep<<<BB, 512, 0, stream>>>(slots, lsg, lsb, Wq, W2, b2, w2q, qb2);
 
     for (int it = 0; it <= NITERS; ++it) {
-        k_slot_prep<<<BB, 512, 0, stream>>>(slots, lsg, lsb, Wq, W2, b2, w2q, qb2);
         k_pass1<<<dim3(64, BB), 256, 0, stream>>>(uk, kaux, positions, scales,
                                                   avec, bvec, s1v, b1p, wgc, w2q, qb2, dots);
-        k_softmax_ms<<<BB * SS, 256, 0, stream>>>(dots, Mv, Lv, H);
-        k_attn<<<dim3(16, BB), 256, 0, stream>>>(dots, Mv, Lv, attn);
+        k_softmax_ms<<<BB * SS, 256, 0, stream>>>(dots, Mv, Lv, H, stats5);
         if (it < NITERS) {
             k_pass2<<<dim3(64, BB), 256, 0, stream>>>(uv, vaux, positions, scales,
-                                                      avec, bvec, s1v, b1p, wgc, attn, H);
-            k_stats<<<BB * SS, 256, 0, stream>>>(attn, gbuf, positions, scales, stats);
-            k_gru_mlp<<<BB * SS, 64, 0, stream>>>(H, stats, W2, b2, W_ih, W_hh, b_ih, b_hh,
-                                                  lmg, lmb, W3, b3, W4, b4, slots);
+                                                      avec, bvec, s1v, b1p, wgc,
+                                                      dots, Mv, Lv, H, stats5);
+            k_gru_fused<<<BB, 512, 0, stream>>>(H, stats5, positions, scales,
+                                                W2, b2, W_ih, W_hh, b_ih, b_hh,
+                                                lmg, lmb, W3, b3, W4, b4,
+                                                lsg, lsb, Wq, slots, w2q, qb2);
         } else {
-            k_stats<<<BB * SS, 256, 0, stream>>>(attn, gbuf, positions, scales, stats);
+            k_stats_final<<<dim3(16, BB), 256, 0, stream>>>(dots, kaux, Mv, Lv, stats5);
+            k_finalize<<<1, 128, 0, stream>>>(stats5, positions, scales);
         }
     }
     k_write_out<<<34, 256, 0, stream>>>(slots, positions, scales, out);
```

Result: slower. 617.3 us (+30.0%).
